# Optimization experiments

Measured on AMD Instinct MI355X. Metric: run time of the kernel, lower is better.

## Reference

```python
import jax, jax.numpy as jnp
import numpy as np

D = 768        # d_model
NH = 12        # n_head
HD = D // NH   # head_dim = 64
T = 8          # num_frames
SCALE = 1.0
LN_EPS = 1e-5


def _layer_norm(x, g, b):
    # fp16-safe LayerNorm: compute in fp32, cast back (matches LayerNorm subclass)
    x32 = x.astype(jnp.float32)
    mu = jnp.mean(x32, axis=-1, keepdims=True)
    var = jnp.mean(jnp.square(x32 - mu), axis=-1, keepdims=True)
    y = (x32 - mu) / jnp.sqrt(var + LN_EPS) * g + b
    return y.astype(x.dtype)


def _adapter(x, w1, b1, w2, b2):
    # Adapter with skip_connect=False: fc1 -> exact GELU -> fc2
    h = jax.nn.gelu(x @ w1.T + b1, approximate=False)
    return h @ w2.T + b2


def _mha(xq, ykv, w_in, b_in, w_out, b_out, need_weights=False):
    # xq: (Tx, N, D), ykv: (Ty, N, D); manual in-proj split like the torch code
    q = xq @ w_in[:D].T + b_in[:D]
    k = ykv @ w_in[D:2 * D].T + b_in[D:2 * D]
    v = ykv @ w_in[2 * D:].T + b_in[2 * D:]
    Tx, N = q.shape[0], q.shape[1]
    Ty = k.shape[0]
    q = q.reshape(Tx, N, NH, HD).transpose(1, 2, 0, 3)  # (N, H, Tx, hd)
    k = k.reshape(Ty, N, NH, HD).transpose(1, 2, 0, 3)
    v = v.reshape(Ty, N, NH, HD).transpose(1, 2, 0, 3)
    aff = jnp.einsum('nhqd,nhkd->nhqk', q, k) / jnp.asarray(HD ** 0.5, q.dtype)
    if need_weights:
        # torch does this under no_grad: sum over heads, exp, sum over (Tx*Ty)
        w = jax.lax.stop_gradient(
            jnp.sum(jnp.exp(jnp.sum(aff, axis=1)).reshape(N, -1), axis=-1))
    p = jax.nn.softmax(aff, axis=-1)
    out = jnp.einsum('nhqk,nhkd->nhqd', p, v)
    out = out.transpose(2, 0, 1, 3).reshape(Tx, N, D)
    out = out @ w_out.T + b_out
    if need_weights:
        return out, w
    return out


def setup_inputs() -> dict:
    key = jax.random.key(0)
    ks = jax.random.split(key, 12)
    DH = D // 4  # adapter hidden = 192

    def w(k, shape):
        return jax.random.normal(k, shape, jnp.float32) * 0.02

    z = lambda *s: jnp.zeros(s, jnp.float32)
    return {
        'x': jax.random.normal(ks[0], (197, 64, D), jnp.float32),
        'in_proj_w': w(ks[1], (3 * D, D)), 'in_proj_b': z(3 * D),
        'out_proj_w': w(ks[2], (D, D)), 'out_proj_b': z(D),
        'ln1_g': jnp.ones((D,), jnp.float32), 'ln1_b': z(D),
        'ln2_g': jnp.ones((D,), jnp.float32), 'ln2_b': z(D),
        'fc_w': w(ks[3], (4 * D, D)), 'fc_b': z(4 * D),
        'proj_w': w(ks[4], (D, 4 * D)), 'proj_b': z(D),
        'sa1_w': w(ks[5], (DH, D)), 'sa1_b': z(DH),
        'sa2_w': w(ks[6], (D, DH)), 'sa2_b': z(D),
        'ta1_w': w(ks[7], (DH, D)), 'ta1_b': z(DH),
        'ta2_w': w(ks[8], (D, DH)), 'ta2_b': z(D),
        'ma1_w': w(ks[9], (DH, D)), 'ma1_b': z(DH),
        'ma2_w': w(ks[10], (D, DH)), 'ma2_b': z(D),
    }


def reference(x, in_proj_w, in_proj_b, out_proj_w, out_proj_b,
              ln1_g, ln1_b, ln2_g, ln2_b, fc_w, fc_b, proj_w, proj_b,
              sa1_w, sa1_b, sa2_w, sa2_b, ta1_w, ta1_b, ta2_w, ta2_b,
              ma1_w, ma1_b, ma2_w, ma2_b):
    n, bt, d = x.shape
    b = bt // T
    # temporal attention on the class token: 'n (b t) d -> t (b n) d'
    ct = x[0]                                   # (bt, d)
    xt = ct.reshape(b, T, d).transpose(1, 0, 2)  # (T, b, d)
    xt = _mha(_layer_norm(xt, ln1_g, ln1_b), _layer_norm(xt, ln1_g, ln1_b),
              in_proj_w, in_proj_b, out_proj_w, out_proj_b)
    xt = _adapter(xt, ta1_w, ta1_b, ta2_w, ta2_b)
    xt = xt.transpose(1, 0, 2).reshape(1, bt, d)  # 't (b n) d -> n (b t) d'

    xln = _layer_norm(x, ln1_g, ln1_b)
    ori_attn, ori_w = _mha(xln, xln, in_proj_w, in_proj_b,
                           out_proj_w, out_proj_b, need_weights=True)
    crs_attn, crs_w = _mha(xln, xt, in_proj_w, in_proj_b,
                           out_proj_w, out_proj_b, need_weights=True)
    lam = (crs_w / (crs_w + ori_w))[None, :, None]  # (1, bt, 1)
    x = x + (1.0 - lam) * ori_attn \
          + SCALE * _adapter(lam * crs_attn, sa1_w, sa1_b, sa2_w, sa2_b)

    xn = _layer_norm(x, ln2_g, ln2_b)
    h = xn @ fc_w.T + fc_b
    h = h * jax.nn.sigmoid(1.702 * h)  # QuickGELU
    mlp_out = h @ proj_w.T + proj_b
    x = x + mlp_out + SCALE * _adapter(xn, ma1_w, ma1_b, ma2_w, ma2_b)
    return x
```

## Files before the change

kernel.cpp:

```cpp
#include <hip/hip_runtime.h>
#include <hip/hip_bf16.h>
#include <math.h>


typedef __attribute__((ext_vector_type(8))) short bf16x8;
typedef __attribute__((ext_vector_type(4))) float f32x4;

__device__ __forceinline__ float bf2f(short s) {
  unsigned u = ((unsigned)(unsigned short)s) << 16;
  float f;
  __builtin_memcpy(&f, &u, 4);
  return f;
}
__device__ __forceinline__ short f2bf(float f) {
  __hip_bfloat16 h = __float2bfloat16(f);
  short s;
  __builtin_memcpy(&s, &h, 2);
  return s;
}

__device__ __forceinline__ void gld16(void* lds, const void* g) {
  __builtin_amdgcn_global_load_lds(
      (const __attribute__((address_space(1))) unsigned int*)g,
      (__attribute__((address_space(3))) unsigned int*)lds, 16, 0, 0);
}

struct WPair { const float* s; short* d; int n; };
struct WArr { WPair p[10]; };

__global__ __launch_bounds__(256)
void convert_k(WArr a) {
  WPair w = a.p[blockIdx.y];
  for (int i = blockIdx.x * 256 + threadIdx.x; i < w.n; i += gridDim.x * 256)
    w.d[i] = f2bf(w.s[i]);
}

__global__ __launch_bounds__(256)
void catf_k(const float* __restrict__ a, const float* __restrict__ b,
            float* __restrict__ o) {
  int i = blockIdx.x * 256 + threadIdx.x;
  if (i < 3328)
    o[i] = i < 3072 ? a[i] : (i < 3264 ? b[i - 3072] : 0.f);
}

__global__ __launch_bounds__(256)
void ln_k(const float* __restrict__ in, const float* __restrict__ g,
          const float* __restrict__ b, short* __restrict__ out) {
  const int t = blockIdx.x;
  const float* xr = in + (size_t)t * 768;
  const int tid = threadIdx.x;
  float v0 = xr[tid], v1 = xr[tid + 256], v2 = xr[tid + 512];
  float s = v0 + v1 + v2;
#pragma unroll
  for (int m = 1; m < 64; m <<= 1) s += __shfl_xor(s, m);
  __shared__ float red[4];
  if ((tid & 63) == 0) red[tid >> 6] = s;
  __syncthreads();
  float mu = (red[0] + red[1] + red[2] + red[3]) * (1.f / 768.f);
  __syncthreads();
  float d0 = v0 - mu, d1 = v1 - mu, d2 = v2 - mu;
  float q = d0 * d0 + d1 * d1 + d2 * d2;
#pragma unroll
  for (int m = 1; m < 64; m <<= 1) q += __shfl_xor(q, m);
  if ((tid & 63) == 0) red[tid >> 6] = q;
  __syncthreads();
  float rstd = rsqrtf((red[0] + red[1] + red[2] + red[3]) * (1.f / 768.f) + 1e-5f);
  size_t o = (size_t)t * 768;
  out[o + tid]       = f2bf(d0 * rstd * g[tid]       + b[tid]);
  out[o + tid + 256] = f2bf(d1 * rstd * g[tid + 256] + b[tid + 256]);
  out[o + tid + 512] = f2bf(d2 * rstd * g[tid + 512] + b[tid + 512]);
}

template <int ACT, int EPI>
__global__ __launch_bounds__(256)
void gemm_k(const short* __restrict__ A, int lda,
            const short* __restrict__ W,
            const float* __restrict__ bias,
            short* __restrict__ outb, float* __restrict__ outf,
            const float* __restrict__ lam,
            int M, int N, int K) {
  __shared__ short As[64][40];
  __shared__ short Ws[64][40];
  const int tid = threadIdx.x;
  const int n0 = blockIdx.x * 64;
  const int m0 = blockIdx.y * 64;
  const int lane = tid & 63, w = tid >> 6;
  const int wr = w >> 1, wc = w & 1;
  const int g = lane >> 4, li = lane & 15;
  const int srow = tid >> 2, scol = (tid & 3) * 8;

  f32x4 acc[2][2];
#pragma unroll
  for (int i = 0; i < 2; i++)
#pragma unroll
    for (int j = 0; j < 2; j++) acc[i][j] = (f32x4){0.f, 0.f, 0.f, 0.f};

  const short* Aptr = A + (size_t)(m0 + srow) * lda + scol;
  const short* Wptr = W + (size_t)(n0 + srow) * K + scol;

  for (int kk = 0; kk < K; kk += 32) {
    __syncthreads();
    *(bf16x8*)&As[srow][scol] = *(const bf16x8*)(Aptr + kk);
    *(bf16x8*)&Ws[srow][scol] = *(const bf16x8*)(Wptr + kk);
    __syncthreads();
    bf16x8 a[2], b[2];
#pragma unroll
    for (int mi = 0; mi < 2; ++mi)
      a[mi] = *(const bf16x8*)&As[wr * 32 + mi * 16 + li][g * 8];
#pragma unroll
    for (int ni = 0; ni < 2; ++ni)
      b[ni] = *(const bf16x8*)&Ws[wc * 32 + ni * 16 + li][g * 8];
#pragma unroll
    for (int mi = 0; mi < 2; ++mi)
#pragma unroll
      for (int ni = 0; ni < 2; ++ni)
        acc[mi][ni] = __builtin_amdgcn_mfma_f32_16x16x32_bf16(
            a[mi], b[ni], acc[mi][ni], 0, 0, 0);
  }

#pragma unroll
  for (int mi = 0; mi < 2; ++mi)
#pragma unroll
    for (int ni = 0; ni < 2; ++ni)
#pragma unroll
      for (int r = 0; r < 4; ++r) {
        int row = m0 + wr * 32 + mi * 16 + g * 4 + r;
        int col = n0 + wc * 32 + ni * 16 + li;
        float v = acc[mi][ni][r];
        if (bias) v += bias[col];
        if (ACT == 1) v = v / (1.f + __expf(-1.702f * v));
        if (ACT == 2) v = 0.5f * v * (1.f + erff(v * 0.70710678118f));
        size_t idx = (size_t)row * N + col;
        if (EPI == 0) outb[idx] = f2bf(v);
        else if (EPI == 1) outf[idx] = v;
        else if (EPI == 5) outb[idx] = f2bf(v * lam[row]);
      }
}

template <int ACT, int EPI>
__global__ __launch_bounds__(512, 4)
void gemm256x128_k(const short* __restrict__ A, int lda,
                   const short* __restrict__ W,
                   const float* __restrict__ bias,
                   short* __restrict__ outb, short* __restrict__ outb2,
                   int M, int N, int NW, int K, int nx) {
  int nwg = gridDim.x;
  int orig = blockIdx.x;
  int q = nwg >> 3, r = nwg & 7;
  int xcd = orig & 7, cidx = orig >> 3;
  int wgid = (xcd < r ? xcd * (q + 1) : r * (q + 1) + (xcd - r) * q) + cidx;
  const int n0 = (wgid % nx) * 128;
  const int m0 = (wgid / nx) * 256;

  __shared__ short As[2][256][32];
  __shared__ short Ws[2][128][32];
  const int tid = threadIdx.x;
  const int w = tid >> 6, lane = tid & 63;
  const int g = lane >> 4, li = lane & 15;
  const int wr = w >> 1, wc = w & 1;

  const int sgc = ((tid & 3) ^ ((tid >> 3) & 3)) * 8;
  const int cxr = (g ^ ((li >> 1) & 3)) * 8;

  f32x4 acc[4][4];
#pragma unroll
  for (int i = 0; i < 4; i++)
#pragma unroll
    for (int j = 0; j < 4; j++) acc[i][j] = (f32x4){0.f, 0.f, 0.f, 0.f};

  int arj[2];
#pragma unroll
  for (int j = 0; j < 2; ++j) {
    int rA = m0 + j * 128 + (tid >> 2);
    arj[j] = rA > M - 1 ? M - 1 : rA;
  }
  int wrow = n0 + (tid >> 2);
  if (wrow > NW - 1) wrow = NW - 1;
  const short* Ap0 = A + (size_t)arj[0] * lda + sgc;
  const short* Ap1 = A + (size_t)arj[1] * lda + sgc;
  const short* Wp  = W + (size_t)wrow * K + sgc;

  const int total = K >> 5;

  auto STAGE = [&](int s, int bi) {
    const int kk = s * 32;
    gld16(&As[bi][w * 16][0],       Ap0 + kk);
    gld16(&As[bi][128 + w * 16][0], Ap1 + kk);
    gld16(&Ws[bi][w * 16][0],       Wp + kk);
  };

  STAGE(0, 0);

  for (int t = 0; t < total; ++t) {
    const int bi = t & 1;
    if (t + 1 < total) {
      STAGE(t + 1, bi ^ 1);
      asm volatile("s_waitcnt vmcnt(3)" ::: "memory");
    } else {
      asm volatile("s_waitcnt vmcnt(0)" ::: "memory");
    }
    __builtin_amdgcn_s_barrier();

    bf16x8 a[4], b[4];
#pragma unroll
    for (int mi = 0; mi < 4; ++mi)
      a[mi] = *(const bf16x8*)&As[bi][wr * 64 + mi * 16 + li][cxr];
#pragma unroll
    for (int ni = 0; ni < 4; ++ni)
      b[ni] = *(const bf16x8*)&Ws[bi][wc * 64 + ni * 16 + li][cxr];
    asm volatile("s_waitcnt lgkmcnt(0)" ::: "memory");
    __builtin_amdgcn_sched_barrier(0);
#pragma unroll
    for (int mi = 0; mi < 4; ++mi)
#pragma unroll
      for (int ni = 0; ni < 4; ++ni)
        acc[mi][ni] = __builtin_amdgcn_mfma_f32_16x16x32_bf16(
            a[mi], b[ni], acc[mi][ni], 0, 0, 0);
    __builtin_amdgcn_s_barrier();
  }

#pragma unroll
  for (int mi = 0; mi < 4; ++mi)
#pragma unroll
    for (int ni = 0; ni < 4; ++ni)
#pragma unroll
      for (int r = 0; r < 4; ++r) {
        int row = m0 + wr * 64 + mi * 16 + g * 4 + r;
        int col = n0 + wc * 64 + ni * 16 + li;
        if (row >= M) continue;
        float v = acc[mi][ni][r];
        if (EPI == 0) {
          if (bias) v += bias[col];
          if (ACT == 1) v = v / (1.f + __expf(-1.702f * v));
          outb[(size_t)row * N + col] = f2bf(v);
        } else {
          if (col < 3072) {
            v += bias[col];
            v = v / (1.f + __expf(-1.702f * v));
            outb[(size_t)row * 3072 + col] = f2bf(v);
          } else if (col < 3264) {
            v += bias[col];
            v = 0.5f * v * (1.f + erff(v * 0.70710678118f));
            outb2[(size_t)row * 192 + (col - 3072)] = f2bf(v);
          }
        }
      }
}

template <int ACT, int EPI>
__global__ __launch_bounds__(512, 6)
void gemm512_k(const short* __restrict__ A, int lda,
               const short* __restrict__ W,
               const float* __restrict__ bias,
               short* __restrict__ outb, float* __restrict__ outf,
               const float* __restrict__ lam,
               const float* __restrict__ addv,
               const float* __restrict__ resid,
               const short* __restrict__ A2, int lda2,
               const short* __restrict__ W2,
               const float* __restrict__ bias2, int K2,
               int M, int N, int K, int nx) {
  int nwg = gridDim.x;
  int orig = blockIdx.x;
  int q = nwg >> 3, r = nwg & 7;
  int xcd = orig & 7, cidx = orig >> 3;
  int wgid = (xcd < r ? xcd * (q + 1) : r * (q + 1) + (xcd - r) * q) + cidx;
  const int n0 = (wgid % nx) * 128;
  const int m0 = (wgid / nx) * 128;

  __shared__ short As[2][128][32];
  __shared__ short Ws[2][128][32];
  const int tid = threadIdx.x;
  const int w = tid >> 6, lane = tid & 63;
  const int g = lane >> 4, li = lane & 15;
  const int wr = w >> 2, wc = w & 3;

  const int srow = tid >> 2;
  const int scol = ((tid & 3) ^ ((tid >> 3) & 3)) * 8;
  const int cxr  = (g ^ ((li >> 1) & 3)) * 8;

  f32x4 acc[4][2];
#pragma unroll
  for (int i = 0; i < 4; i++)
#pragma unroll
    for (int j = 0; j < 2; j++) acc[i][j] = (f32x4){0.f, 0.f, 0.f, 0.f};

  int ar = m0 + srow; if (ar > M - 1) ar = M - 1;
  const short* Ap = A + (size_t)ar * lda + scol;
  const short* Wp = W + (size_t)(n0 + srow) * K + scol;
  const short* A2b = A2 ? A2 : A;
  const short* W2b = W2 ? W2 : W;
  const short* Bp = A2b + (size_t)ar * lda2 + scol;
  const short* Vp = W2b + (size_t)(n0 + srow) * K2 + scol;

  const int ks1 = K >> 5;
  const int ks2 = A2 ? (K2 >> 5) : 0;
  const int total = ks1 + ks2;

  auto STAGE = [&](int s, int bi) {
    if (s < ks1) {
      const int kk = s * 32;
      gld16(&As[bi][w * 16][0], Ap + kk);
      gld16(&Ws[bi][w * 16][0], Wp + kk);
    } else {
      const int kk = (s - ks1) * 32;
      gld16(&As[bi][w * 16][0], Bp + kk);
      gld16(&Ws[bi][w * 16][0], Vp + kk);
    }
  };

  STAGE(0, 0);

  for (int t = 0; t < total; ++t) {
    const int bi = t & 1;
    if (t + 1 < total) {
      STAGE(t + 1, bi ^ 1);
      asm volatile("s_waitcnt vmcnt(2)" ::: "memory");
    } else {
      asm volatile("s_waitcnt vmcnt(0)" ::: "memory");
    }
    __builtin_amdgcn_s_barrier();

    bf16x8 a[4], b[2];
#pragma unroll
    for (int mi = 0; mi < 4; ++mi)
      a[mi] = *(const bf16x8*)&As[bi][wr * 64 + mi * 16 + li][cxr];
#pragma unroll
    for (int ni = 0; ni < 2; ++ni)
      b[ni] = *(const bf16x8*)&Ws[bi][wc * 32 + ni * 16 + li][cxr];
    asm volatile("s_waitcnt lgkmcnt(0)" ::: "memory");
    __builtin_amdgcn_sched_barrier(0);
#pragma unroll
    for (int mi = 0; mi < 4; ++mi)
#pragma unroll
      for (int ni = 0; ni < 2; ++ni)
        acc[mi][ni] = __builtin_amdgcn_mfma_f32_16x16x32_bf16(
            a[mi], b[ni], acc[mi][ni], 0, 0, 0);
    __builtin_amdgcn_s_barrier();
  }

#pragma unroll
  for (int mi = 0; mi < 4; ++mi)
#pragma unroll
    for (int ni = 0; ni < 2; ++ni)
#pragma unroll
      for (int r = 0; r < 4; ++r) {
        int row = m0 + wr * 64 + mi * 16 + g * 4 + r;
        int col = n0 + wc * 32 + ni * 16 + li;
        if (row >= M) continue;
        float v = acc[mi][ni][r];
        if (bias) v += bias[col];
        if (bias2) v += bias2[col];
        if (ACT == 1) v = v / (1.f + __expf(-1.702f * v));
        if (ACT == 2) v = 0.5f * v * (1.f + erff(v * 0.70710678118f));
        size_t idx = (size_t)row * N + col;
        if (EPI == 0) outb[idx] = f2bf(v);
        else if (EPI == 2) {
          float l = lam[row & 63];
          outf[idx] = resid[idx] + (1.f - l) * v + addv[(size_t)(row & 63) * 768 + col];
        } else if (EPI == 6) outf[idx] = resid[idx] + v;
      }
}

__global__ __launch_bounds__(256)
void attn_k(const short* __restrict__ qkv, short* __restrict__ attn_out) {
  const int n = blockIdx.x;
  const int h = blockIdx.y;
  const int tid = threadIdx.x;
  const int lane = tid & 63, w = tid >> 6;
  const int g = lane >> 4, li = lane & 15;

  __shared__ short Vt[64][232];
  __shared__ short Pl[4][16][232];

  {
    const int d = tid & 63;
    for (int key = tid >> 6; key < 224; key += 4) {
      short v = 0;
      if (key < 197)
        v = qkv[(size_t)(key * 64 + n) * 2304 + 1536 + h * 64 + d];
      Vt[d][key] = v;
    }
  }
  __syncthreads();

  const short* Qb = qkv + (size_t)n * 2304 + h * 64;
  const short* Kb = Qb + 768;

  for (int mt = w; mt < 13; mt += 4) {
    const int m0 = mt * 16;
    int arow = m0 + li;
    if (arow > 196) arow = 196;
    bf16x8 a0 = *(const bf16x8*)(Qb + (size_t)arow * 147456 + g * 8);
    bf16x8 a1 = *(const bf16x8*)(Qb + (size_t)arow * 147456 + 32 + g * 8);

    float s[13][4];
#pragma unroll
    for (int nt = 0; nt < 13; ++nt) {
      int kc = nt * 16 + li;
      if (kc > 196) kc = 196;
      bf16x8 b0 = *(const bf16x8*)(Kb + (size_t)kc * 147456 + g * 8);
      bf16x8 b1 = *(const bf16x8*)(Kb + (size_t)kc * 147456 + 32 + g * 8);
      f32x4 acc = (f32x4){0.f, 0.f, 0.f, 0.f};
      acc = __builtin_amdgcn_mfma_f32_16x16x32_bf16(a0, b0, acc, 0, 0, 0);
      acc = __builtin_amdgcn_mfma_f32_16x16x32_bf16(a1, b1, acc, 0, 0, 0);
#pragma unroll
      for (int r = 0; r < 4; ++r) s[nt][r] = acc[r] * 0.125f;
    }

#pragma unroll
    for (int r = 0; r < 4; ++r) {
      float mx = -1e30f;
#pragma unroll
      for (int nt = 0; nt < 13; ++nt) {
        if (nt * 16 + li >= 197) s[nt][r] = -1e30f;
        mx = fmaxf(mx, s[nt][r]);
      }
      mx = fmaxf(mx, __shfl_xor(mx, 1));
      mx = fmaxf(mx, __shfl_xor(mx, 2));
      mx = fmaxf(mx, __shfl_xor(mx, 4));
      mx = fmaxf(mx, __shfl_xor(mx, 8));
      float sum = 0.f;
#pragma unroll
      for (int nt = 0; nt < 13; ++nt) {
        float e = (s[nt][r] <= -1e29f) ? 0.f : __expf(s[nt][r] - mx);
        s[nt][r] = e;
        sum += e;
      }
      sum += __shfl_xor(sum, 1);
      sum += __shfl_xor(sum, 2);
      sum += __shfl_xor(sum, 4);
      sum += __shfl_xor(sum, 8);
      float inv = 1.f / sum;
#pragma unroll
      for (int nt = 0; nt < 13; ++nt) s[nt][r] *= inv;
    }

#pragma unroll
    for (int r = 0; r < 4; ++r) {
      int row = g * 4 + r;
#pragma unroll
      for (int nt = 0; nt < 13; ++nt)
        Pl[w][row][nt * 16 + li] = f2bf(s[nt][r]);
      Pl[w][row][208 + li] = 0;
    }
    asm volatile("s_waitcnt lgkmcnt(0)" ::: "memory");
    __builtin_amdgcn_sched_barrier(0);

    f32x4 o[4];
#pragma unroll
    for (int ni = 0; ni < 4; ++ni) o[ni] = (f32x4){0.f, 0.f, 0.f, 0.f};
#pragma unroll
    for (int kk = 0; kk < 7; ++kk) {
      bf16x8 pa = *(const bf16x8*)&Pl[w][li][kk * 32 + g * 8];
#pragma unroll
      for (int ni = 0; ni < 4; ++ni) {
        bf16x8 vb = *(const bf16x8*)&Vt[ni * 16 + li][kk * 32 + g * 8];
        o[ni] = __builtin_amdgcn_mfma_f32_16x16x32_bf16(pa, vb, o[ni], 0, 0, 0);
      }
    }
#pragma unroll
    for (int ni = 0; ni < 4; ++ni)
#pragma unroll
      for (int r = 0; r < 4; ++r) {
        int prow = m0 + g * 4 + r;
        if (prow < 197)
          attn_out[(size_t)(prow * 64 + n) * 768 + h * 64 + ni * 16 + li] =
              f2bf(o[ni][r]);
      }
  }
}

__global__ __launch_bounds__(256)
void lam_part_k(const short* __restrict__ qkv, float* __restrict__ eo_part) {
  const int n = blockIdx.x;
  const int mt = blockIdx.y;
  const int tid = threadIdx.x;
  const int lane = tid & 63, w = tid >> 6;
  const int g = lane >> 4, li = lane & 15;
  const short* Qb = qkv + (size_t)n * 2304;
  const short* Kb = Qb + 768;

  int arow = mt * 16 + li;
  if (arow > 196) arow = 196;
  const short* Ap = Qb + (size_t)arow * 147456;

  bf16x8 a[24];
#pragma unroll
  for (int s = 0; s < 24; ++s)
    a[s] = *(const bf16x8*)(Ap + s * 32 + g * 8);

  float eo = 0.f;
  for (int nt = w; nt < 13; nt += 4) {
    int kc = nt * 16 + li;
    if (kc > 196) kc = 196;
    const short* Bp = Kb + (size_t)kc * 147456;
    f32x4 acc = (f32x4){0.f, 0.f, 0.f, 0.f};
#pragma unroll
    for (int s = 0; s < 24; ++s) {
      bf16x8 b = *(const bf16x8*)(Bp + s * 32 + g * 8);
      acc = __builtin_amdgcn_mfma_f32_16x16x32_bf16(a[s], b, acc, 0, 0, 0);
    }
#pragma unroll
    for (int r = 0; r < 4; ++r) {
      int prow = mt * 16 + g * 4 + r;
      int col = nt * 16 + li;
      if (prow < 197 && col < 197) eo += __expf(acc[r] * 0.125f);
    }
  }

#pragma unroll
  for (int m = 1; m < 64; m <<= 1) eo += __shfl_xor(eo, m);
  __shared__ float red[4];
  if (lane == 0) red[w] = eo;
  __syncthreads();
  if (tid == 0)
    eo_part[n * 13 + mt] = red[0] + red[1] + red[2] + red[3];
}

__global__ __launch_bounds__(64)
void lam_fin_k(const short* __restrict__ qkv, const short* __restrict__ kvt,
               const float* __restrict__ eo_part, float* __restrict__ lam) {
  const int n = blockIdx.x;
  const int lane = threadIdx.x;
  const short* kt = kvt + (size_t)n * 1536;

  float ec = 0.f;
  for (int p = lane; p < 197; p += 64) {
    const short* qp = qkv + (size_t)n * 2304 + (size_t)p * 147456;
    float dot = 0.f;
    for (int d0 = 0; d0 < 768; d0 += 8) {
      bf16x8 qa = *(const bf16x8*)(qp + d0);
      bf16x8 ka = *(const bf16x8*)(kt + d0);
#pragma unroll
      for (int j = 0; j < 8; ++j) dot += bf2f(qa[j]) * bf2f(ka[j]);
    }
    ec += __expf(dot * 0.125f);
  }
#pragma unroll
  for (int m = 1; m < 64; m <<= 1) ec += __shfl_xor(ec, m);

  if (lane == 0) {
    float eo = 0.f;
#pragma unroll
    for (int t = 0; t < 13; ++t) eo += eo_part[n * 13 + t];
    lam[n] = ec / (ec + eo);
  }
}

__global__ __launch_bounds__(64)
void tattn_k(const short* __restrict__ qkv, short* __restrict__ attn_t) {
  const int bb = blockIdx.x, h = blockIdx.y;
  const int tid = threadIdx.x;
  __shared__ float sm[8][9];
  {
    const int tt = tid >> 3, ss = tid & 7;
    const short* q = qkv + (size_t)(bb * 8 + tt) * 2304 + h * 64;
    const short* k = qkv + (size_t)(bb * 8 + ss) * 2304 + 768 + h * 64;
    float dot = 0.f;
#pragma unroll
    for (int d = 0; d < 64; d += 8) {
      bf16x8 qa = *(const bf16x8*)(q + d);
      bf16x8 ka = *(const bf16x8*)(k + d);
#pragma unroll
      for (int j = 0; j < 8; ++j) dot += bf2f(qa[j]) * bf2f(ka[j]);
    }
    sm[tt][ss] = dot * 0.125f;
  }
  __syncthreads();
  if (tid < 8) {
    float mx = -1e30f;
#pragma unroll
    for (int s2 = 0; s2 < 8; ++s2) mx = fmaxf(mx, sm[tid][s2]);
    float sum = 0.f;
#pragma unroll
    for (int s2 = 0; s2 < 8; ++s2) {
      float e = __expf(sm[tid][s2] - mx);
      sm[tid][s2] = e;
      sum += e;
    }
    float inv = 1.f / sum;
#pragma unroll
    for (int s2 = 0; s2 < 8; ++s2) sm[tid][s2] *= inv;
  }
  __syncthreads();
  {
    const int d = tid;
    float v[8];
#pragma unroll
    for (int s2 = 0; s2 < 8; ++s2)
      v[s2] = bf2f(qkv[(size_t)(bb * 8 + s2) * 2304 + 1536 + h * 64 + d]);
#pragma unroll
    for (int tt = 0; tt < 8; ++tt) {
      float o = 0.f;
#pragma unroll
      for (int s2 = 0; s2 < 8; ++s2) o += sm[tt][s2] * v[s2];
      attn_t[(size_t)(bb * 8 + tt) * 768 + h * 64 + d] = f2bf(o);
    }
  }
}

extern "C" void kernel_launch(void* const* d_in, const int* in_sizes, int n_in,
                              void* d_out, int out_size, void* d_ws,
                              size_t ws_size, hipStream_t stream) {
  (void)in_sizes; (void)n_in; (void)out_size; (void)ws_size;

  const float* x          = (const float*)d_in[0];
  const float* in_proj_w  = (const float*)d_in[1];
  const float* in_proj_b  = (const float*)d_in[2];
  const float* out_proj_w = (const float*)d_in[3];
  const float* out_proj_b = (const float*)d_in[4];
  const float* ln1_g      = (const float*)d_in[5];
  const float* ln1_b      = (const float*)d_in[6];
  const float* ln2_g      = (const float*)d_in[7];
  const float* ln2_b      = (const float*)d_in[8];
  const float* fc_w       = (const float*)d_in[9];
  const float* fc_b       = (const float*)d_in[10];
  const float* proj_w     = (const float*)d_in[11];
  const float* proj_b     = (const float*)d_in[12];
  const float* sa1_w      = (const float*)d_in[13];
  const float* sa1_b      = (const float*)d_in[14];
  const float* sa2_w      = (const float*)d_in[15];
  const float* sa2_b      = (const float*)d_in[16];
  const float* ta1_w      = (const float*)d_in[17];
  const float* ta1_b      = (const float*)d_in[18];
  const float* ta2_w      = (const float*)d_in[19];
  const float* ta2_b      = (const float*)d_in[20];
  const float* ma1_w      = (const float*)d_in[21];
  const float* ma1_b      = (const float*)d_in[22];
  const float* ma2_w      = (const float*)d_in[23];
  const float* ma2_b      = (const float*)d_in[24];

  char* ws = (char*)d_ws;
  short* xln  = (short*)(ws + 0);
  short* qkv  = (short*)(ws + 19365888);
  short* hbuf = (short*)(ws + 0);
  short* attn = (short*)(ws + 77463552);
  short* h2   = (short*)(ws + 77463552);
  float* x1   = (float*)(ws + 96829440);
  short* xn   = (short*)(ws + 135561216);

  char* wreg = ws + 154927104;
  short* w_inproj  = (short*)(wreg + 0);
  short* w_outproj = (short*)(wreg + 3538944);
  short* w_fcma    = (short*)(wreg + 4718592);
  short* w_proj    = (short*)(wreg + 9732096);
  short* w_sa1     = (short*)(wreg + 14450688);
  short* w_sa2     = (short*)(wreg + 14745600);
  short* w_ta1     = (short*)(wreg + 15040512);
  short* w_ta2     = (short*)(wreg + 15335424);
  short* w_ma2     = (short*)(wreg + 15630336);
  float* cbias     = (float*)(wreg + 15925248);

  char* sm = ws + 171966464;
  short* attn_t  = (short*)(sm + 0);
  short* tproj   = (short*)(sm + 98304);
  short* th      = (short*)(sm + 196608);
  short* xt_out  = (short*)(sm + 221184);
  short* kv_t    = (short*)(sm + 319488);
  short* a_in    = (short*)(sm + 516096);
  short* sa_h    = (short*)(sm + 614400);
  float* sa_out  = (float*)(sm + 638976);
  float* lam     = (float*)(sm + 835584);
  float* eo_part = (float*)(sm + 835840);

  float* out = (float*)d_out;

  WArr arr;
  arr.p[0] = {in_proj_w,  w_inproj,            2304 * 768};
  arr.p[1] = {out_proj_w, w_outproj,           768 * 768};
  arr.p[2] = {fc_w,       w_fcma,              3072 * 768};
  arr.p[3] = {proj_w,     w_proj,              768 * 3072};
  arr.p[4] = {sa1_w,      w_sa1,               192 * 768};
  arr.p[5] = {sa2_w,      w_sa2,               768 * 192};
  arr.p[6] = {ta1_w,      w_ta1,               192 * 768};
  arr.p[7] = {ta2_w,      w_ta2,               768 * 192};
  arr.p[8] = {ma1_w,      w_fcma + 3072 * 768, 192 * 768};
  arr.p[9] = {ma2_w,      w_ma2,               768 * 192};
  convert_k<<<dim3(128, 10), 256, 0, stream>>>(arr);
  catf_k<<<13, 256, 0, stream>>>(fc_b, ma1_b, cbias);

  ln_k<<<12608, 256, 0, stream>>>(x, ln1_g, ln1_b, xln);

  gemm256x128_k<0, 0><<<50 * 18, 512, 0, stream>>>(
      xln, 768, w_inproj, in_proj_b, qkv, nullptr, 12608, 2304, 2304, 768, 18);

  lam_part_k<<<dim3(64, 13), 256, 0, stream>>>(qkv, eo_part);

  tattn_k<<<dim3(8, 12), 64, 0, stream>>>(qkv, attn_t);

  gemm_k<0, 0><<<dim3(12, 1), 256, 0, stream>>>(
      attn_t, 768, w_outproj, out_proj_b, tproj, nullptr, nullptr, 64, 768, 768);
  gemm_k<2, 0><<<dim3(3, 1), 256, 0, stream>>>(
      tproj, 768, w_ta1, ta1_b, th, nullptr, nullptr, 64, 192, 768);
  gemm_k<0, 0><<<dim3(12, 1), 256, 0, stream>>>(
      th, 192, w_ta2, ta2_b, xt_out, nullptr, nullptr, 64, 768, 192);
  gemm_k<0, 0><<<dim3(24, 1), 256, 0, stream>>>(
      xt_out, 768, w_inproj + 768 * 768, in_proj_b + 768, kv_t, nullptr,
      nullptr, 64, 1536, 768);

  attn_k<<<dim3(64, 12), 256, 0, stream>>>(qkv, attn);

  lam_fin_k<<<64, 64, 0, stream>>>(qkv, kv_t, eo_part, lam);

  gemm_k<0, 5><<<dim3(12, 1), 256, 0, stream>>>(
      kv_t + 768, 1536, w_outproj, out_proj_b, a_in, nullptr, lam, 64, 768, 768);
  gemm_k<2, 0><<<dim3(3, 1), 256, 0, stream>>>(
      a_in, 768, w_sa1, sa1_b, sa_h, nullptr, nullptr, 64, 192, 768);
  gemm_k<0, 1><<<dim3(12, 1), 256, 0, stream>>>(
      sa_h, 192, w_sa2, sa2_b, nullptr, sa_out, nullptr, 64, 768, 192);

  gemm512_k<0, 2><<<6 * 99, 512, 0, stream>>>(
      attn, 768, w_outproj, out_proj_b, nullptr, x1, lam, sa_out, x,
      nullptr, 0, nullptr, nullptr, 32, 12608, 768, 768, 6);

  ln_k<<<12608, 256, 0, stream>>>(x1, ln2_g, ln2_b, xn);

  gemm256x128_k<1, 7><<<50 * 26, 512, 0, stream>>>(
      xn, 768, w_fcma, cbias, hbuf, h2, 12608, 3328, 3264, 768, 26);

  gemm512_k<0, 6><<<6 * 99, 512, 0, stream>>>(
      hbuf, 3072, w_proj, proj_b, nullptr, out, nullptr, nullptr, x1,
      h2, 192, w_ma2, ma2_b, 192, 12608, 768, 3072, 6);
}
```

Measured before the change: 628.4 us.

## Fuse small temporal-attention and adapter GEMM chain into one cooperative kernel

Replaces nine small launches (temporal attention, the tiny M=64 GEMMs of the temporal and spatial adapter chains, and the lambda finalisation) with a single 24-block cooperative kernel that uses grid-wide syncs between stages. The aim is to remove per-launch overhead and idle gaps on a chain of tiny dependent kernels. In exchange, the whole chain now runs on only 24 workgroups, each stage is separated by a grid barrier, and the ACT/EPI choices become runtime parameters instead of template arguments. This fused chain still runs after the large attention kernel rather than overlapping it.

```diff
diff --git a/kernel.cpp b/kernel.cpp
--- a/kernel.cpp
+++ b/kernel.cpp
@@ -1,6 +1,9 @@
 #include <hip/hip_runtime.h>
 #include <hip/hip_bf16.h>
+#include <hip/hip_cooperative_groups.h>
 #include <math.h>
+
+namespace cg = cooperative_groups;
 
 
 typedef __attribute__((ext_vector_type(8))) short bf16x8;
@@ -71,19 +74,11 @@
   out[o + tid + 512] = f2bf(d2 * rstd * g[tid + 512] + b[tid + 512]);
 }
 
-template <int ACT, int EPI>
-__global__ __launch_bounds__(256)
-void gemm_k(const short* __restrict__ A, int lda,
-            const short* __restrict__ W,
-            const float* __restrict__ bias,
-            short* __restrict__ outb, float* __restrict__ outf,
-            const float* __restrict__ lam,
-            int M, int N, int K) {
-  __shared__ short As[64][40];
-  __shared__ short Ws[64][40];
+__device__ void g64(const short* A, int lda, const short* W,
+                    const float* bias, short* outb, float* outf,
+                    const float* lam, int n0, int N, int K, int ACT, int EPI,
+                    short (*As)[40], short (*Ws)[40]) {
   const int tid = threadIdx.x;
-  const int n0 = blockIdx.x * 64;
-  const int m0 = blockIdx.y * 64;
   const int lane = tid & 63, w = tid >> 6;
   const int wr = w >> 1, wc = w & 1;
   const int g = lane >> 4, li = lane & 15;
@@ -95,7 +90,7 @@
 #pragma unroll
     for (int j = 0; j < 2; j++) acc[i][j] = (f32x4){0.f, 0.f, 0.f, 0.f};
 
-  const short* Aptr = A + (size_t)(m0 + srow) * lda + scol;
+  const short* Aptr = A + (size_t)srow * lda + scol;
   const short* Wptr = W + (size_t)(n0 + srow) * K + scol;
 
   for (int kk = 0; kk < K; kk += 32) {
@@ -124,17 +119,156 @@
     for (int ni = 0; ni < 2; ++ni)
 #pragma unroll
       for (int r = 0; r < 4; ++r) {
-        int row = m0 + wr * 32 + mi * 16 + g * 4 + r;
+        int row = wr * 32 + mi * 16 + g * 4 + r;
         int col = n0 + wc * 32 + ni * 16 + li;
         float v = acc[mi][ni][r];
         if (bias) v += bias[col];
         if (ACT == 1) v = v / (1.f + __expf(-1.702f * v));
-        if (ACT == 2) v = 0.5f * v * (1.f + erff(v * 0.70710678118f));
+        else if (ACT == 2) v = 0.5f * v * (1.f + erff(v * 0.70710678118f));
         size_t idx = (size_t)row * N + col;
         if (EPI == 0) outb[idx] = f2bf(v);
         else if (EPI == 1) outf[idx] = v;
         else if (EPI == 5) outb[idx] = f2bf(v * lam[row]);
       }
+}
+
+struct CoopArgs {
+  const short* qkv;
+  const short* w_outproj; const float* out_proj_b;
+  const short* w_ta1;     const float* ta1_b;
+  const short* w_ta2;     const float* ta2_b;
+  const short* w_inproj768; const float* in_proj_b768;
+  const short* w_sa1;     const float* sa1_b;
+  const short* w_sa2;     const float* sa2_b;
+  const float* eo_part;
+  short* attn_t; short* tproj; short* th; short* xt_out; short* kv_t;
+  short* a_in; short* sa_h; float* sa_out; float* lam;
+};
+
+__global__ __launch_bounds__(256)
+void coop_k(CoopArgs a) {
+  cg::grid_group grid = cg::this_grid();
+  __shared__ short As[64][40];
+  __shared__ short Ws[64][40];
+  __shared__ float sm4[4][8][9];
+  __shared__ float redc[4];
+  const int b = blockIdx.x, tid = threadIdx.x;
+  const int lane = tid & 63, w = tid >> 6;
+
+  {
+    const int pair = b * 4 + (tid >> 6);
+    const int bb = pair / 12, h = pair % 12;
+    const int l = tid & 63;
+    float (*sm)[9] = sm4[tid >> 6];
+    {
+      const int tt = l >> 3, ss = l & 7;
+      const short* q = a.qkv + (size_t)(bb * 8 + tt) * 2304 + h * 64;
+      const short* k = a.qkv + (size_t)(bb * 8 + ss) * 2304 + 768 + h * 64;
+      float dot = 0.f;
+#pragma unroll
+      for (int d = 0; d < 64; d += 8) {
+        bf16x8 qa = *(const bf16x8*)(q + d);
+        bf16x8 ka = *(const bf16x8*)(k + d);
+#pragma unroll
+        for (int j = 0; j < 8; ++j) dot += bf2f(qa[j]) * bf2f(ka[j]);
+      }
+      sm[tt][ss] = dot * 0.125f;
+    }
+    __syncthreads();
+    if (l < 8) {
+      float mx = -1e30f;
+#pragma unroll
+      for (int s2 = 0; s2 < 8; ++s2) mx = fmaxf(mx, sm[l][s2]);
+      float sum = 0.f;
+#pragma unroll
+      for (int s2 = 0; s2 < 8; ++s2) {
+        float e = __expf(sm[l][s2] - mx);
+        sm[l][s2] = e;
+        sum += e;
+      }
+      float inv = 1.f / sum;
+#pragma unroll
+      for (int s2 = 0; s2 < 8; ++s2) sm[l][s2] *= inv;
+    }
+    __syncthreads();
+    {
+      const int d = l;
+      float v[8];
+#pragma unroll
+      for (int s2 = 0; s2 < 8; ++s2)
+        v[s2] = bf2f(a.qkv[(size_t)(bb * 8 + s2) * 2304 + 1536 + h * 64 + d]);
+#pragma unroll
+      for (int tt = 0; tt < 8; ++tt) {
+        float o = 0.f;
+#pragma unroll
+        for (int s2 = 0; s2 < 8; ++s2) o += sm[tt][s2] * v[s2];
+        a.attn_t[(size_t)(bb * 8 + tt) * 768 + h * 64 + d] = f2bf(o);
+      }
+    }
+  }
+  grid.sync();
+
+  if (b < 12)
+    g64(a.attn_t, 768, a.w_outproj, a.out_proj_b, a.tproj, nullptr, nullptr,
+        b * 64, 768, 768, 0, 0, As, Ws);
+  grid.sync();
+
+  if (b < 3)
+    g64(a.tproj, 768, a.w_ta1, a.ta1_b, a.th, nullptr, nullptr,
+        b * 64, 192, 768, 2, 0, As, Ws);
+  grid.sync();
+
+  if (b < 12)
+    g64(a.th, 192, a.w_ta2, a.ta2_b, a.xt_out, nullptr, nullptr,
+        b * 64, 768, 192, 0, 0, As, Ws);
+  grid.sync();
+
+  g64(a.xt_out, 768, a.w_inproj768, a.in_proj_b768, a.kv_t, nullptr, nullptr,
+      b * 64, 1536, 768, 0, 0, As, Ws);
+  grid.sync();
+
+  for (int n = b; n < 64; n += 24) {
+    const short* kt = a.kv_t + (size_t)n * 1536;
+    float ec = 0.f;
+    for (int p = tid; p < 197; p += 256) {
+      const short* qp = a.qkv + (size_t)n * 2304 + (size_t)p * 147456;
+      float dot = 0.f;
+      for (int d0 = 0; d0 < 768; d0 += 8) {
+        bf16x8 qa = *(const bf16x8*)(qp + d0);
+        bf16x8 ka = *(const bf16x8*)(kt + d0);
+#pragma unroll
+        for (int j = 0; j < 8; ++j) dot += bf2f(qa[j]) * bf2f(ka[j]);
+      }
+      ec += __expf(dot * 0.125f);
+    }
+#pragma unroll
+    for (int m = 1; m < 64; m <<= 1) ec += __shfl_xor(ec, m);
+    if (lane == 0) redc[w] = ec;
+    __syncthreads();
+    if (tid == 0) {
+      float Ec = redc[0] + redc[1] + redc[2] + redc[3];
+      float eo = 0.f;
+#pragma unroll
+      for (int t = 0; t < 13; ++t) eo += a.eo_part[n * 13 + t];
+      a.lam[n] = Ec / (Ec + eo);
+    }
+    __syncthreads();
+  }
+  grid.sync();
+
+  if (b < 12)
+    g64(a.kv_t + 768, 1536, a.w_outproj, a.out_proj_b, a.a_in, nullptr, a.lam,
+        b * 64, 768, 768, 0, 5, As, Ws);
+  grid.sync();
+
+  if (b < 3)
+    g64(a.a_in, 768, a.w_sa1, a.sa1_b, a.sa_h, nullptr, nullptr,
+        b * 64, 192, 768, 2, 0, As, Ws);
+  grid.sync();
+
+  if (b < 12)
+    g64(a.sa_h, 192, a.w_sa2, a.sa2_b, nullptr, a.sa_out, nullptr,
+        b * 64, 768, 192, 0, 1, As, Ws);
 }
 
 template <int ACT, int EPI>
@@ -516,88 +650,6 @@
   __syncthreads();
   if (tid == 0)
     eo_part[n * 13 + mt] = red[0] + red[1] + red[2] + red[3];
-}
-
-__global__ __launch_bounds__(64)
-void lam_fin_k(const short* __restrict__ qkv, const short* __restrict__ kvt,
-               const float* __restrict__ eo_part, float* __restrict__ lam) {
-  const int n = blockIdx.x;
-  const int lane = threadIdx.x;
-  const short* kt = kvt + (size_t)n * 1536;
-
-  float ec = 0.f;
-  for (int p = lane; p < 197; p += 64) {
-    const short* qp = qkv + (size_t)n * 2304 + (size_t)p * 147456;
-    float dot = 0.f;
-    for (int d0 = 0; d0 < 768; d0 += 8) {
-      bf16x8 qa = *(const bf16x8*)(qp + d0);
-      bf16x8 ka = *(const bf16x8*)(kt + d0);
-#pragma unroll
-      for (int j = 0; j < 8; ++j) dot += bf2f(qa[j]) * bf2f(ka[j]);
-    }
-    ec += __expf(dot * 0.125f);
-  }
-#pragma unroll
-  for (int m = 1; m < 64; m <<= 1) ec += __shfl_xor(ec, m);
-
-  if (lane == 0) {
-    float eo = 0.f;
-#pragma unroll
-    for (int t = 0; t < 13; ++t) eo += eo_part[n * 13 + t];
-    lam[n] = ec / (ec + eo);
-  }
-}
-
-__global__ __launch_bounds__(64)
-void tattn_k(const short* __restrict__ qkv, short* __restrict__ attn_t) {
-  const int bb = blockIdx.x, h = blockIdx.y;
-  const int tid = threadIdx.x;
-  __shared__ float sm[8][9];
-  {
-    const int tt = tid >> 3, ss = tid & 7;
-    const short* q = qkv + (size_t)(bb * 8 + tt) * 2304 + h * 64;
-    const short* k = qkv + (size_t)(bb * 8 + ss) * 2304 + 768 + h * 64;
-    float dot = 0.f;
-#pragma unroll
-    for (int d = 0; d < 64; d += 8) {
-      bf16x8 qa = *(const bf16x8*)(q + d);
-      bf16x8 ka = *(const bf16x8*)(k + d);
-#pragma unroll
-      for (int j = 0; j < 8; ++j) dot += bf2f(qa[j]) * bf2f(ka[j]);
-    }
-    sm[tt][ss] = dot * 0.125f;
-  }
-  __syncthreads();
-  if (tid < 8) {
-    float mx = -1e30f;
-#pragma unroll
-    for (int s2 = 0; s2 < 8; ++s2) mx = fmaxf(mx, sm[tid][s2]);
-    float sum = 0.f;
-#pragma unroll
-    for (int s2 = 0; s2 < 8; ++s2) {
-      float e = __expf(sm[tid][s2] - mx);
-      sm[tid][s2] = e;
-      sum += e;
-    }
-    float inv = 1.f / sum;
-#pragma unroll
-    for (int s2 = 0; s2 < 8; ++s2) sm[tid][s2] *= inv;
-  }
-  __syncthreads();
-  {
-    const int d = tid;
-    float v[8];
-#pragma unroll
-    for (int s2 = 0; s2 < 8; ++s2)
-      v[s2] = bf2f(qkv[(size_t)(bb * 8 + s2) * 2304 + 1536 + h * 64 + d]);
-#pragma unroll
-    for (int tt = 0; tt < 8; ++tt) {
-      float o = 0.f;
-#pragma unroll
-      for (int s2 = 0; s2 < 8; ++s2) o += sm[tt][s2] * v[s2];
-      attn_t[(size_t)(bb * 8 + tt) * 768 + h * 64 + d] = f2bf(o);
-    }
-  }
 }
 
 extern "C" void kernel_launch(void* const* d_in, const int* in_sizes, int n_in,
@@ -687,28 +739,24 @@
 
   lam_part_k<<<dim3(64, 13), 256, 0, stream>>>(qkv, eo_part);
 
-  tattn_k<<<dim3(8, 12), 64, 0, stream>>>(qkv, attn_t);
-
-  gemm_k<0, 0><<<dim3(12, 1), 256, 0, stream>>>(
-      attn_t, 768, w_outproj, out_proj_b, tproj, nullptr, nullptr, 64, 768, 768);
-  gemm_k<2, 0><<<dim3(3, 1), 256, 0, stream>>>(
-      tproj, 768, w_ta1, ta1_b, th, nullptr, nullptr, 64, 192, 768);
-  gemm_k<0, 0><<<dim3(12, 1), 256, 0, stream>>>(
-      th, 192, w_ta2, ta2_b, xt_out, nullptr, nullptr, 64, 768, 192);
-  gemm_k<0, 0><<<dim3(24, 1), 256, 0, stream>>>(
-      xt_out, 768, w_inproj + 768 * 768, in_proj_b + 768, kv_t, nullptr,
-      nullptr, 64, 1536, 768);
-
   attn_k<<<dim3(64, 12), 256, 0, stream>>>(qkv, attn);
 
-  lam_fin_k<<<64, 64, 0, stream>>>(qkv, kv_t, eo_part, lam);
-
-  gemm_k<0, 5><<<dim3(12, 1), 256, 0, stream>>>(
-      kv_t + 768, 1536, w_outproj, out_proj_b, a_in, nullptr, lam, 64, 768, 768);
-  gemm_k<2, 0><<<dim3(3, 1), 256, 0, stream>>>(
-      a_in, 768, w_sa1, sa1_b, sa_h, nullptr, nullptr, 64, 192, 768);
-  gemm_k<0, 1><<<dim3(12, 1), 256, 0, stream>>>(
-      sa_h, 192, w_sa2, sa2_b, nullptr, sa_out, nullptr, 64, 768, 192);
+  CoopArgs ca;
+  ca.qkv = qkv;
+  ca.w_outproj = w_outproj;          ca.out_proj_b = out_proj_b;
+  ca.w_ta1 = w_ta1;                  ca.ta1_b = ta1_b;
+  ca.w_ta2 = w_ta2;                  ca.ta2_b = ta2_b;
+  ca.w_inproj768 = w_inproj + 768 * 768;
+  ca.in_proj_b768 = in_proj_b + 768;
+  ca.w_sa1 = w_sa1;                  ca.sa1_b = sa1_b;
+  ca.w_sa2 = w_sa2;                  ca.sa2_b = sa2_b;
+  ca.eo_part = eo_part;
+  ca.attn_t = attn_t; ca.tproj = tproj; ca.th = th; ca.xt_out = xt_out;
+  ca.kv_t = kv_t; ca.a_in = a_in; ca.sa_h = sa_h; ca.sa_out = sa_out;
+  ca.lam = lam;
+  void* kargs[] = {(void*)&ca};
+  hipLaunchCooperativeKernel((void*)coop_k, dim3(24), dim3(256), kargs, 0,
+                             stream);
 
   gemm512_k<0, 2><<<6 * 99, 512, 0, stream>>>(
       attn, 768, w_outproj, out_proj_b, nullptr, x1, lam, sa_out, x,
```

Measured after the change: 685.8 us. +9.1%, slower.
